# Kernel optimization log

Measured on AMD Instinct MI355X. Metric: run time of the kernel, lower is better.

The kernel has to match this reference:

```python
import jax, jax.numpy as jnp
import numpy as np

C = 32  # channel dim ('size' in the torch module)


def setup_inputs() -> dict:
    key = jax.random.key(0)
    ks = jax.random.split(key, 9)
    B, H, W = 8, 64, 512
    shape = (B, C, H, W)
    q = jax.random.normal(ks[0], shape, dtype=jnp.float32)
    k = jax.random.normal(ks[1], shape, dtype=jnp.float32)
    v = jax.random.normal(ks[2], shape, dtype=jnp.float32)
    s = 1.0 / np.sqrt(C)  # kaiming-uniform-ish scale for 1x1 conv
    wq = jax.random.uniform(ks[3], (C, C), jnp.float32, -s, s)
    bq = jax.random.uniform(ks[4], (C,), jnp.float32, -s, s)
    wk = jax.random.uniform(ks[5], (C, C), jnp.float32, -s, s)
    bk = jax.random.uniform(ks[6], (C,), jnp.float32, -s, s)
    wv = jax.random.uniform(ks[7], (C, C), jnp.float32, -s, s)
    bv = jax.random.uniform(ks[8], (C,), jnp.float32, -s, s)
    return {"q": q, "k": k, "v": v, "wq": wq, "bq": bq,
            "wk": wk, "bk": bk, "wv": wv, "bv": bv}


def _proj(x, w, b):
    # 1x1 conv on NCHW == per-pixel linear over channels; emit NHWC directly
    return jnp.einsum('oc,bchw->bhwo', w, x) + b


def reference(q, k, v, wq, bq, wk, bk, wv, bv):
    residual = q  # [B,C,H,W]
    qp = _proj(q, wq, bq)  # [B,H,W,C]
    kp = _proj(k, wk, bk)
    vp = _proj(v, wv, bv)
    # unnormalized attention over the W axis, batched over (B,H)
    attn = jnp.einsum('bhwc,bhxc->bhwx', qp, kp)        # [B,H,W,W]
    att = jnp.einsum('bhwx,bhxc->bhwc', attn, vp)       # [B,H,W,C]
    out = jnp.transpose(att, (0, 3, 1, 2)) + residual   # back to NCHW
    return out
```

## Files before the change

### kernel.cpp

```cpp
#include <hip/hip_runtime.h>
#include <hip/hip_bf16.h>

#define CH   32
#define WD   512
#define NH   64
#define CHST (NH * WD)
#define BST  (CH * CHST)
#define NST  36

typedef short bf16x8 __attribute__((ext_vector_type(8)));
typedef float f32x16 __attribute__((ext_vector_type(16)));
typedef float f32x8  __attribute__((ext_vector_type(8)));

__device__ __forceinline__ unsigned short f2bf(float f) {
  union { __hip_bfloat16 h; unsigned short u; } cv;
  cv.h = __float2bfloat16(f);
  return cv.u;
}
__device__ __forceinline__ float bf2f(unsigned short u) {
  return __uint_as_float(((unsigned int)u) << 16);
}
__device__ __forceinline__ unsigned int pk2(float lo_, float hi_) {
  return ((unsigned int)f2bf(hi_) << 16) | (unsigned int)f2bf(lo_);
}
__device__ __forceinline__ void swap32(unsigned int& a, unsigned int& b) {
  asm volatile("v_permlane32_swap_b32 %0, %1" : "+v"(a), "+v"(b));
}
union W4 { unsigned int u[4]; bf16x8 v; };

__device__ __forceinline__ void d2frag(const f32x16& d, W4& f0, W4& f1) {
  f0.u[0] = pk2(d[0], d[1]);   f0.u[1] = pk2(d[2],  d[3]);
  f0.u[2] = pk2(d[4], d[5]);   f0.u[3] = pk2(d[6],  d[7]);
  swap32(f0.u[0], f0.u[2]);    swap32(f0.u[1], f0.u[3]);
  f1.u[0] = pk2(d[8], d[9]);   f1.u[1] = pk2(d[10], d[11]);
  f1.u[2] = pk2(d[12], d[13]); f1.u[3] = pk2(d[14], d[15]);
  swap32(f1.u[0], f1.u[2]);    swap32(f1.u[1], f1.u[3]);
}
__device__ __forceinline__ float halfsum(float v) {
  unsigned int a = __float_as_uint(v), b = a;
  swap32(a, b);
  return __uint_as_float(a) + __uint_as_float(b);
}

__global__ __launch_bounds__(512, 4)
void fused_mha(const float* __restrict__ qg, const float* __restrict__ kg,
               const float* __restrict__ vg,
               const float* __restrict__ wqg, const float* __restrict__ bqg,
               const float* __restrict__ wkg, const float* __restrict__ bkg,
               const float* __restrict__ wvg, const float* __restrict__ bvg,
               float* __restrict__ outg)
{
  __shared__ float np[8][CH][NST];
  __shared__ float sp[8][2][CH];

  const int t = threadIdx.x, lane = t & 63, wid = t >> 6;
  const int lo = lane & 31, hi = lane >> 5;
  const int bh = blockIdx.x;
  const size_t base = (size_t)(bh >> 6) * BST + (size_t)(bh & 63) * WD;

  int rowr[16];
  #pragma unroll
  for (int r = 0; r < 16; ++r) rowr[r] = (r & 3) + 8 * (r >> 2) + 4 * hi;

  bf16x8 wkA[2], wvA[2];
  {
    const float* wk_r = wkg + lo * CH + 8 * hi;
    const float* wv_r = wvg + lo * CH + 8 * hi;
    #pragma unroll
    for (int s = 0; s < 2; ++s)
      #pragma unroll
      for (int j = 0; j < 8; ++j) {
        wkA[s][j] = (short)f2bf(wk_r[16 * s + j]);
        wvA[s][j] = (short)f2bf(wv_r[16 * s + j]);
      }
  }

  const float* krow = kg + base + (size_t)lo * CHST + 64 * wid + 8 * hi;
  const float* vrow = vg + base + (size_t)lo * CHST + 64 * wid + 8 * hi;
  f32x8 kf[4], vf[4];
  #pragma unroll
  for (int kk = 0; kk < 4; ++kk) {
    kf[kk] = *(const f32x8*)(krow + 16 * kk);
    vf[kk] = *(const f32x8*)(vrow + 16 * kk);
  }
  f32x16 nacc;
  #pragma unroll
  for (int r = 0; r < 16; ++r) nacc[r] = 0.f;
  float psK = 0.f, psV = 0.f;
  #pragma unroll
  for (int kk = 0; kk < 4; ++kk) {
    W4 kb, vb;
    #pragma unroll
    for (int i = 0; i < 4; ++i) {
      kb.u[i] = pk2(kf[kk][2 * i], kf[kk][2 * i + 1]);
      vb.u[i] = pk2(vf[kk][2 * i], vf[kk][2 * i + 1]);
    }
    nacc = __builtin_amdgcn_mfma_f32_32x32x16_bf16(kb.v, vb.v, nacc, 0, 0, 0);
    #pragma unroll
    for (int j = 0; j < 8; ++j) { psK += kf[kk][j]; psV += vf[kk][j]; }
  }
  #pragma unroll
  for (int r = 0; r < 16; ++r) np[wid][rowr[r]][lo] = nacc[r];
  {
    const float sk = halfsum(psK), sv = halfsum(psV);
    if (hi == 0) { sp[wid][0][lo] = sk; sp[wid][1][lo] = sv; }
  }
  __syncthreads();

  {
    #pragma unroll
    for (int p = 0; p < 2; ++p) {
      const int e = t + 512 * p, o = e >> 5, c = e & 31;
      float s = 0.f;
      #pragma unroll
      for (int w = 0; w < 8; ++w) s += np[w][o][c];
      np[0][o][c] = s;
    }
    if (t < 64) {
      const int j = t >> 5, o = t & 31;
      float s = 0.f;
      #pragma unroll
      for (int w = 0; w < 8; ++w) s += sp[w][j][o];
      sp[0][j][o] = s;
    }
  }
  __syncthreads();

  float qpf[32];
  #pragma unroll
  for (int it = 0; it < 2; ++it)
    #pragma unroll
    for (int s = 0; s < 2; ++s)
      #pragma unroll
      for (int j = 0; j < 8; ++j)
        qpf[16 * it + 8 * s + j] =
            qg[base + (size_t)(16 * s + 8 * hi + j) * CHST + 64 * wid + 32 * it + lo];

  bf16x8 wqA[2];
  {
    #pragma unroll
    for (int s = 0; s < 2; ++s)
      #pragma unroll
      for (int j = 0; j < 8; ++j)
        wqA[s][j] = (short)f2bf(wqg[(16 * s + 8 * hi + j) * CH + lo]);
  }
  float bkr[16], bqr[16];
  #pragma unroll
  for (int r = 0; r < 16; ++r) { bkr[r] = bkg[rowr[r]]; bqr[r] = bqg[rowr[r]]; }
  const float bvlo = bvg[lo];

  W4 NAh[2], NAl[2];
  #pragma unroll
  for (int s = 0; s < 2; ++s) {
    f32x8 nf = *(const f32x8*)&np[0][lo][16 * s + 8 * hi];
    #pragma unroll
    for (int i = 0; i < 4; ++i) {
      const float x = nf[2 * i], y = nf[2 * i + 1];
      const unsigned short hx = f2bf(x), hy = f2bf(y);
      NAh[s].u[i] = ((unsigned int)hy << 16) | hx;
      NAl[s].u[i] = pk2(x - bf2f(hx), y - bf2f(hy));
    }
  }
  f32x16 pacc;
  #pragma unroll
  for (int r = 0; r < 16; ++r) pacc[r] = 0.f;
  pacc = __builtin_amdgcn_mfma_f32_32x32x16_bf16(NAh[0].v, wvA[0], pacc, 0, 0, 0);
  pacc = __builtin_amdgcn_mfma_f32_32x32x16_bf16(NAh[1].v, wvA[1], pacc, 0, 0, 0);
  pacc = __builtin_amdgcn_mfma_f32_32x32x16_bf16(NAl[0].v, wvA[0], pacc, 0, 0, 0);
  pacc = __builtin_amdgcn_mfma_f32_32x32x16_bf16(NAl[1].v, wvA[1], pacc, 0, 0, 0);
  f32x16 pp;
  #pragma unroll
  for (int r = 0; r < 16; ++r) pp[r] = pacc[r] + sp[0][0][rowr[r]] * bvlo;
  float uprt = 0.f;
  #pragma unroll
  for (int s = 0; s < 2; ++s)
    #pragma unroll
    for (int j = 0; j < 8; ++j)
      uprt += bf2f((unsigned short)wvA[s][j]) * sp[0][1][16 * s + 8 * hi + j];
  const float uful = halfsum(uprt) + 512.f * bvlo;
  f32x16 pres;
  #pragma unroll
  for (int r = 0; r < 16; ++r) pres[r] = pp[r] - bf2f(f2bf(pp[r]));
  W4 pb0h, pb1h, pb0l, pb1l;
  d2frag(pp, pb0h, pb1h);
  d2frag(pres, pb0l, pb1l);
  f32x16 mac;
  #pragma unroll
  for (int r = 0; r < 16; ++r) mac[r] = bkr[r] * uful;
  mac = __builtin_amdgcn_mfma_f32_32x32x16_bf16(wkA[0], pb0h.v, mac, 0, 0, 0);
  mac = __builtin_amdgcn_mfma_f32_32x32x16_bf16(wkA[1], pb1h.v, mac, 0, 0, 0);
  mac = __builtin_amdgcn_mfma_f32_32x32x16_bf16(wkA[0], pb0l.v, mac, 0, 0, 0);
  mac = __builtin_amdgcn_mfma_f32_32x32x16_bf16(wkA[1], pb1l.v, mac, 0, 0, 0);
  W4 mb0, mb1;
  d2frag(mac, mb0, mb1);
  f32x16 gacc;
  #pragma unroll
  for (int r = 0; r < 16; ++r) gacc[r] = 0.f;
  gacc = __builtin_amdgcn_mfma_f32_32x32x16_bf16(wqA[0], mb0.v, gacc, 0, 0, 0);
  gacc = __builtin_amdgcn_mfma_f32_32x32x16_bf16(wqA[1], mb1.v, gacc, 0, 0, 0);
  #pragma unroll
  for (int r = 0; r < 16; ++r)
    if (rowr[r] == lo) gacc[r] += 1.f;
  float part = 0.f;
  #pragma unroll
  for (int r = 0; r < 16; ++r) part = fmaf(bqr[r], mac[r], part);
  const float gv = halfsum(part);
  W4 ga0, ga1;
  d2frag(gacc, ga0, ga1);
  float gsh[16];
  #pragma unroll
  for (int r = 0; r < 16; ++r) gsh[r] = __shfl(gv, rowr[r], 64);

  #pragma unroll
  for (int it = 0; it < 2; ++it) {
    const int x0 = 64 * wid + 32 * it;
    bf16x8 qb[2];
    #pragma unroll
    for (int s = 0; s < 2; ++s)
      #pragma unroll
      for (int j = 0; j < 8; ++j)
        qb[s][j] = (short)f2bf(qpf[16 * it + 8 * s + j]);
    f32x16 acc;
    #pragma unroll
    for (int r = 0; r < 16; ++r) acc[r] = gsh[r];
    acc = __builtin_amdgcn_mfma_f32_32x32x16_bf16(ga0.v, qb[0], acc, 0, 0, 0);
    acc = __builtin_amdgcn_mfma_f32_32x32x16_bf16(ga1.v, qb[1], acc, 0, 0, 0);
    #pragma unroll
    for (int r = 0; r < 16; ++r)
      outg[base + (size_t)rowr[r] * CHST + x0 + lo] = acc[r];
  }
}

extern "C" void kernel_launch(void* const* d_in, const int* in_sizes, int n_in,
                              void* d_out, int out_size, void* d_ws, size_t ws_size,
                              hipStream_t stream) {
  const float* q  = (const float*)d_in[0];
  const float* k  = (const float*)d_in[1];
  const float* v  = (const float*)d_in[2];
  const float* wq = (const float*)d_in[3];
  const float* bq = (const float*)d_in[4];
  const float* wk = (const float*)d_in[5];
  const float* bk = (const float*)d_in[6];
  const float* wv = (const float*)d_in[7];
  const float* bv = (const float*)d_in[8];
  float* out = (float*)d_out;

  (void)in_sizes; (void)n_in; (void)out_size; (void)d_ws; (void)ws_size;

  fused_mha<<<dim3(8 * 64), dim3(512), 0, stream>>>(q, k, v, wq, bq, wk, bk, wv, bv, out);
}
```

Measured before the change: 29.30 us.

## Split each row's output across two blocks and prefetch q before barrier

The grid doubles so that two blocks handle each (batch,row) pair. Each block still recomputes the full K^T V and column sums over all 512 positions but produces output for only half of the W positions. The q loads move ahead of the reduction barrier so their latency overlaps the shared-memory reduction, and halfsum uses a lane-xor shuffle in place of permlane swap. This trades redundant K/V reads and compute for more blocks across CUs and shorter per-block tails.

Result: slower. 40.04 us (+36.7%).

```diff
diff --git a/kernel.cpp b/kernel.cpp
--- a/kernel.cpp
+++ b/kernel.cpp
@@ -37,9 +37,7 @@
   swap32(f1.u[0], f1.u[2]);    swap32(f1.u[1], f1.u[3]);
 }
 __device__ __forceinline__ float halfsum(float v) {
-  unsigned int a = __float_as_uint(v), b = a;
-  swap32(a, b);
-  return __uint_as_float(a) + __uint_as_float(b);
+  return v + __shfl_xor(v, 32, 64);
 }
 
 __global__ __launch_bounds__(512, 4)
@@ -55,7 +53,8 @@
 
   const int t = threadIdx.x, lane = t & 63, wid = t >> 6;
   const int lo = lane & 31, hi = lane >> 5;
-  const int bh = blockIdx.x;
+  const int bid = blockIdx.x;
+  const int bh = bid >> 1, half = bid & 1;
   const size_t base = (size_t)(bh >> 6) * BST + (size_t)(bh & 63) * WD;
 
   int rowr[16];
@@ -105,6 +104,15 @@
     const float sk = halfsum(psK), sv = halfsum(psV);
     if (hi == 0) { sp[wid][0][lo] = sk; sp[wid][1][lo] = sv; }
   }
+
+  float qpf[16];
+  #pragma unroll
+  for (int s = 0; s < 2; ++s)
+    #pragma unroll
+    for (int j = 0; j < 8; ++j)
+      qpf[8 * s + j] = qg[base + (size_t)(16 * s + 8 * hi + j) * CHST +
+                          256 * half + 32 * wid + lo];
+
   __syncthreads();
 
   {
@@ -117,24 +125,14 @@
       np[0][o][c] = s;
     }
     if (t < 64) {
-      const int j = t >> 5, o = t & 31;
-      float s = 0.f;
-      #pragma unroll
-      for (int w = 0; w < 8; ++w) s += sp[w][j][o];
-      sp[0][j][o] = s;
+      const int j = t >> 5, oo = t & 31;
+      float s2 = 0.f;
+      #pragma unroll
+      for (int w = 0; w < 8; ++w) s2 += sp[w][j][oo];
+      sp[0][j][oo] = s2;
     }
   }
   __syncthreads();
-
-  float qpf[32];
-  #pragma unroll
-  for (int it = 0; it < 2; ++it)
-    #pragma unroll
-    for (int s = 0; s < 2; ++s)
-      #pragma unroll
-      for (int j = 0; j < 8; ++j)
-        qpf[16 * it + 8 * s + j] =
-            qg[base + (size_t)(16 * s + 8 * hi + j) * CHST + 64 * wid + 32 * it + lo];
 
   bf16x8 wqA[2];
   {
@@ -211,15 +209,14 @@
   #pragma unroll
   for (int r = 0; r < 16; ++r) gsh[r] = __shfl(gv, rowr[r], 64);
 
-  #pragma unroll
-  for (int it = 0; it < 2; ++it) {
-    const int x0 = 64 * wid + 32 * it;
+  {
+    const int x0 = 256 * half + 32 * wid;
     bf16x8 qb[2];
     #pragma unroll
     for (int s = 0; s < 2; ++s)
       #pragma unroll
       for (int j = 0; j < 8; ++j)
-        qb[s][j] = (short)f2bf(qpf[16 * it + 8 * s + j]);
+        qb[s][j] = (short)f2bf(qpf[8 * s + j]);
     f32x16 acc;
     #pragma unroll
     for (int r = 0; r < 16; ++r) acc[r] = gsh[r];
@@ -247,5 +244,5 @@
 
   (void)in_sizes; (void)n_in; (void)out_size; (void)d_ws; (void)ws_size;
 
-  fused_mha<<<dim3(8 * 64), dim3(512), 0, stream>>>(q, k, v, wq, bq, wk, bk, wv, bv, out);
-}
+  fused_mha<<<dim3(2 * 8 * 64), dim3(512), 0, stream>>>(q, k, v, wq, bq, wk, bk, wv, bv, out);
+}
```
